# Optimization experiments

Hardware: AMD Instinct MI355X
Metric: run time of the kernel (lower is better)

## Reference

```python
import jax, jax.numpy as jnp
import numpy as np

N, E, D = 20000, 640000, 128  # nodes, edges, hidden_nf
ED = 3  # edge_feat_nf (1 input col + distance col + geodesic col)
NORM_FACTOR = 100.0
NORM_CONST = 1.0
LN_EPS = 1e-5


def setup_inputs() -> dict:
    key = jax.random.key(0)
    ks = jax.random.split(key, 24)
    w = lambda k, s: (jax.random.normal(k, s, dtype=jnp.float32) * 0.1)
    inp = {
        "h": jax.random.normal(ks[0], (N, D), dtype=jnp.float32),
        "x": jax.random.normal(ks[1], (N, 3), dtype=jnp.float32),
        "edge_index": jax.random.randint(ks[2], (2, E), 0, N),
        "node_mask": jnp.ones((N, 1), jnp.float32),
        "edge_mask": jnp.ones((E, 1), jnp.float32),
        "edge_attr": jax.random.uniform(ks[3], (E, 1), dtype=jnp.float32),
        # GCLayer params
        "W_lin": w(ks[4], (D, D)), "b_lin": jnp.zeros((D,), jnp.float32),
        "We1": w(ks[5], (D + ED, D)), "be1": jnp.zeros((D,), jnp.float32),
        "We2": w(ks[6], (D, D)), "be2": jnp.zeros((D,), jnp.float32),
        "Wn1": w(ks[7], (D, D)), "bn1": jnp.zeros((D,), jnp.float32),
        "Wn2": w(ks[8], (D, D)), "bn2": jnp.zeros((D,), jnp.float32),
        "Wa1": w(ks[9], (2 * D + ED, D)), "ba1": jnp.zeros((D,), jnp.float32),
        "Wa2": w(ks[10], (D, 1)), "ba2": jnp.zeros((1,), jnp.float32),
        "ln_g": jnp.ones((D,), jnp.float32), "ln_b": jnp.zeros((D,), jnp.float32),
        # EquivariantUpdate coord_mlp params (last layer bias-free, gain 0.001)
        "Wc1": w(ks[11], (2 * D + ED, D)), "bc1": jnp.zeros((D,), jnp.float32),
        "Wc2": w(ks[12], (D, D)), "bc2": jnp.zeros((D,), jnp.float32),
        "Wc3": w(ks[13], (D, 1)) * 0.01,
    }
    return inp


def _forward(h, x, edge_index, node_mask, edge_mask, edge_attr,
             W_lin, b_lin, We1, be1, We2, be2, Wn1, bn1, Wn2, bn2,
             Wa1, ba1, Wa2, ba2, ln_g, ln_b, Wc1, bc1, Wc2, bc2, Wc3):
    silu = jax.nn.silu
    row, col = edge_index[0], edge_index[1]
    # coord2diff
    diff = x[row] - x[col]                                     # [E,3]
    radial = jnp.sum(diff * diff, axis=1, keepdims=True)
    dist = jnp.sqrt(radial + 1e-8)                             # [E,1]
    coord_diff = diff / (dist + NORM_CONST)
    e = jnp.concatenate([dist, edge_attr], axis=1)             # [E,2]
    # ---- GCLayer (Euclidean reduction of HGCLayer) ----
    hh = h @ W_lin + b_lin                                     # [N,D]
    hr, hc = hh[row], hh[col]
    geo = jnp.sqrt(jnp.sum((hr - hc) ** 2, axis=1, keepdims=True) + 1e-8)
    e3 = jnp.concatenate([e, geo], axis=1)                     # [E,3]
    att_in = jnp.concatenate([hr, hc, e3], axis=1)             # [E,2D+3]
    att = jax.nn.sigmoid(silu(att_in @ Wa1 + ba1) @ Wa2 + ba2) * edge_mask
    msg_in = jnp.concatenate([hc - hr, e3], axis=1)            # [E,D+3]
    msg = (silu(msg_in @ We1 + be1) @ We2 + be2) * att
    agg = jax.ops.segment_sum(msg, row, num_segments=hh.shape[0])  # [N,D]
    out = silu(agg @ Wn1 + bn1) @ Wn2 + bn2
    hh = hh + out
    mu = jnp.mean(hh, axis=-1, keepdims=True)
    var = jnp.mean((hh - mu) ** 2, axis=-1, keepdims=True)
    hh = (hh - mu) * jax.lax.rsqrt(var + LN_EPS) * ln_g + ln_b
    hh = silu(hh)
    # ---- EquivariantUpdate (tanh=False) ----
    cin = jnp.concatenate([hh[row], hh[col], e3], axis=1)      # [E,2D+3]
    m = silu(cin @ Wc1 + bc1)
    m = silu(m @ Wc2 + bc2)
    m = m @ Wc3                                                # [E,1]
    trans = coord_diff * m * edge_mask
    aggx = jax.ops.segment_sum(trans, row, num_segments=x.shape[0]) / NORM_FACTOR
    x_out = (x + aggx) * node_mask
    return hh, x_out


def reference(h, x, edge_index, node_mask, edge_mask, edge_attr,
              W_lin, b_lin, We1, be1, We2, be2, Wn1, bn1, Wn2, bn2,
              Wa1, ba1, Wa2, ba2, ln_g, ln_b, Wc1, bc1, Wc2, bc2, Wc3):
    return _forward(h, x, edge_index, node_mask, edge_mask, edge_attr,
                    W_lin, b_lin, We1, be1, We2, be2, Wn1, bn1, Wn2, bn2,
                    Wa1, ba1, Wa2, ba2, ln_g, ln_b, Wc1, bc1, Wc2, bc2, Wc3)
```

## Files before the change

### kernel.cpp

```cpp
#include <hip/hip_runtime.h>
#include <hip/hip_bf16.h>


#define D 128
#define RS 136

typedef unsigned short ushort;
typedef __fp16 half8 __attribute__((ext_vector_type(8)));
typedef __fp16 h16x2 __attribute__((ext_vector_type(2)));
typedef _Float16 f16x2 __attribute__((ext_vector_type(2)));
typedef __attribute__((ext_vector_type(4))) float f32x4;

__device__ __forceinline__ float rcpf(float x) { return __builtin_amdgcn_rcpf(x); }
__device__ __forceinline__ float siluf(float x) { return x * rcpf(1.0f + __expf(-x)); }
__device__ __forceinline__ float sigmf(float x) { return rcpf(1.0f + __expf(-x)); }
__device__ __forceinline__ ushort f2hs(float f) {
    _Float16 h = (_Float16)f; ushort u; __builtin_memcpy(&u, &h, 2); return u;
}
__device__ __forceinline__ unsigned pkh(float lo, float hi) {
    auto h = __builtin_amdgcn_cvt_pkrtz(lo, hi);
    unsigned u; __builtin_memcpy(&u, &h, 4); return u;
}
__device__ __forceinline__ unsigned pkadd(unsigned a, unsigned b) {
    f16x2 x, y; __builtin_memcpy(&x, &a, 4); __builtin_memcpy(&y, &b, 4);
    f16x2 d = x + y; unsigned r; __builtin_memcpy(&r, &d, 4); return r;
}
__device__ __forceinline__ float2 up2(unsigned u) {
    f16x2 h; __builtin_memcpy(&h, &u, 4);
    return make_float2((float)h.x, (float)h.y);
}
__device__ __forceinline__ float fdot2f(f16x2 a, f16x2 b, float c) {
#if __has_builtin(__builtin_amdgcn_fdot2)
    h16x2 ah, bh;
    __builtin_memcpy(&ah, &a, 4); __builtin_memcpy(&bh, &b, 4);
    return __builtin_amdgcn_fdot2(ah, bh, c, false);
#else
    return c + (float)a.x * (float)b.x + (float)a.y * (float)b.y;
#endif
}
#define MFMA16(a, b, c) __builtin_amdgcn_mfma_f32_16x16x32_f16((a), (b), (c), 0, 0, 0)

#define PWLIN 0
#define PU    5
#define PV    9
#define PM    13
#define PE2   17
#define PN1   21
#define PN2   26
#define PP    30
#define PQ    34
#define PC2   38
#define NPACK 42

__global__ void k_zero(float* __restrict__ p, long n) {
    long i = (long)blockIdx.x * blockDim.x + threadIdx.x;
    long stride = (long)gridDim.x * blockDim.x;
    for (; i < n; i += stride) p[i] = 0.0f;
}

__global__ void k_hist(const int* __restrict__ eidx, int* __restrict__ cnt, int E) {
    int i = blockIdx.x * blockDim.x + threadIdx.x;
    const int stride = gridDim.x * blockDim.x;
    for (; i < E; i += stride) atomicAdd(&cnt[eidx[i]], 1);
}

__global__ __launch_bounds__(1024) void k_scan(const int* __restrict__ cnt,
                                               int* __restrict__ cur, int N) {
    __shared__ int part[1024];
    const int t = threadIdx.x;
    const int chunk = (N + 1023) / 1024;
    int s = 0;
    for (int k = 0; k < chunk; ++k) {
        const int i = t * chunk + k;
        if (i < N) s += cnt[i];
    }
    part[t] = s;
    __syncthreads();
    for (int d = 1; d < 1024; d <<= 1) {
        const int v = (t >= d) ? part[t - d] : 0;
        __syncthreads();
        part[t] += v;
        __syncthreads();
    }
    int base = (t == 0) ? 0 : part[t - 1];
    for (int k = 0; k < chunk; ++k) {
        const int i = t * chunk + k;
        if (i < N) { cur[i] = base; base += cnt[i]; }
    }
}

__global__ void k_scatter_build(
    const int* __restrict__ eidx, const float* __restrict__ x,
    const float* __restrict__ eattr, const float* __restrict__ emask,
    int* __restrict__ cur, float4* __restrict__ rec, int E) {
    int i = blockIdx.x * blockDim.x + threadIdx.x;
    const int stride = gridDim.x * blockDim.x;
    for (; i < E; i += stride) {
        const int r = eidx[i], c = eidx[E + i];
        const int p = atomicAdd(&cur[r], 1);
        const float dx = x[r * 3 + 0] - x[c * 3 + 0];
        const float dy = x[r * 3 + 1] - x[c * 3 + 1];
        const float dz = x[r * 3 + 2] - x[c * 3 + 2];
        const float dist = sqrtf(dx * dx + dy * dy + dz * dz + 1e-8f);
        const float inv = rcpf(dist + 1.0f);
        rec[2 * p + 0] = make_float4(__int_as_float(r), __int_as_float(c), dist, eattr[i]);
        rec[2 * p + 1] = make_float4(emask[i], dx * inv, dy * inv, dz * inv);
    }
}

__global__ __launch_bounds__(256) void k_packall(
    const float* __restrict__ W_lin, const float* __restrict__ b_lin,
    const float* __restrict__ Wa1,
    const float* __restrict__ We1,
    const float* __restrict__ We2,
    const float* __restrict__ Wn1, const float* __restrict__ bn1,
    const float* __restrict__ Wn2,
    const float* __restrict__ Wc1,
    const float* __restrict__ Wc2,
    ushort* __restrict__ pack) {
    const int b = blockIdx.x, t = threadIdx.x;
    const float* W = nullptr; const float* bias = nullptr;
    int kbase = 0, fold = 0, ext = 0, nW = 0;
    if (b < 5)       { W = W_lin; bias = b_lin; if (b == 4) { ext = 1; nW = 0; } else kbase = b * 32; }
    else if (b < 9)  { W = Wa1; kbase = (b - 5) * 32; }
    else if (b < 13) { W = Wa1; kbase = 128 + (b - 9) * 32; }
    else if (b < 17) { W = We1; kbase = (b - 13) * 32; }
    else if (b < 21) { W = We2; kbase = (b - 17) * 32; }
    else if (b < 26) { int k = b - 21; W = Wn1; bias = bn1; if (k == 4) { ext = 1; nW = 0; } else kbase = k * 32; }
    else if (b < 30) { W = Wn2; kbase = (b - 26) * 32; }
    else if (b < 34) { W = Wc1; kbase = (b - 30) * 32; }
    else if (b < 38) { W = Wc1; kbase = 128 + (b - 34) * 32; }
    else             { W = Wc2; kbase = (b - 38) * 32; }
    ushort* dst = pack + (size_t)b * 4096;
#pragma unroll
    for (int i = 0; i < 16; ++i) {
        const int e = t + 256 * i;
        const int j = e & 7, lane = (e >> 3) & 63, nt = e >> 9;
        const int kl = (lane >> 4) * 8 + j;
        const int n = nt * 16 + (lane & 15);
        float v;
        if (!ext) {
            v = W[(kbase + kl) * D + n];
            if (fold) v += W[(kbase + kl + 128) * D + n];
        } else {
            v = (kl < nW) ? W[(kbase + kl) * D + n] : (kl == nW ? bias[n] : 0.0f);
        }
        dst[e] = f2hs(v);
    }
}

__global__ __launch_bounds__(256) void k_node_lin(
    const float* __restrict__ h, const ushort* __restrict__ pack,
    float* __restrict__ hh, ushort* __restrict__ hh1b,
    ushort* __restrict__ Vp, ushort* __restrict__ Vh,
    ushort* __restrict__ Mp, ushort* __restrict__ Mh,
    const float* __restrict__ ba1f, const float* __restrict__ be1f, int N) {
    __shared__ ushort hs[64][RS];
    const int t = threadIdx.x, lane = t & 63, wave = t >> 6;
    const int quad = lane >> 4, l16 = lane & 15;
    const int mh = wave >> 1, nh = wave & 1;
    const int base = blockIdx.x * 64;

#pragma unroll
    for (int q = 0; q < 8; ++q) {
        const int f = t + 256 * q;
        const int row = f >> 5, c4 = (f & 31) << 2;
        const int node = base + row;
        float4 v = make_float4(0.f, 0.f, 0.f, 0.f);
        if (node < N) v = *(const float4*)(h + (size_t)node * D + c4);
        *(uint2*)&hs[row][c4] = make_uint2(pkh(v.x, v.y), pkh(v.z, v.w));
    }
    float ba1v[4], be1v[4];
#pragma unroll
    for (int nt = 0; nt < 4; ++nt) {
        const int col = nh * 64 + nt * 16 + l16;
        ba1v[nt] = ba1f[col]; be1v[nt] = be1f[col];
    }
    __syncthreads();

    half8 aext = (half8)0;
    if (quad == 0) aext[0] = (__fp16)1.0f;

    f32x4 acc[2][4] = {};
    {
        const half8* pB = (const half8*)(pack + (size_t)PWLIN * 4096);
#pragma unroll
        for (int ks = 0; ks < 5; ++ks) {
            half8 bfr[4];
#pragma unroll
            for (int nt = 0; nt < 4; ++nt) bfr[nt] = pB[(ks * 8 + nh * 4 + nt) * 64 + lane];
#pragma unroll
            for (int mt = 0; mt < 2; ++mt) {
                const half8 a = (ks < 4) ? *(const half8*)&hs[mh * 32 + mt * 16 + l16][ks * 32 + quad * 8]
                                         : aext;
#pragma unroll
                for (int nt = 0; nt < 4; ++nt) acc[mt][nt] = MFMA16(a, bfr[nt], acc[mt][nt]);
            }
        }
    }
    __syncthreads();
#pragma unroll
    for (int mt = 0; mt < 2; ++mt)
#pragma unroll
        for (int reg = 0; reg < 4; ++reg) {
            const int row = mh * 32 + mt * 16 + quad * 4 + reg;
            const int g = base + row;
#pragma unroll
            for (int nt = 0; nt < 4; ++nt) {
                const int col = nh * 64 + nt * 16 + l16;
                const float v = acc[mt][nt][reg];
                const ushort hv = f2hs(v);
                hs[row][col] = hv;
                if (g < N) {
                    hh[(size_t)g * D + col] = v;
                    hh1b[(size_t)g * D + col] = hv;
                }
            }
        }
    __syncthreads();

    {
        f32x4 a2[2][4] = {};
        const half8* pB = (const half8*)(pack + (size_t)PU * 4096);
#pragma unroll
        for (int ks = 0; ks < 4; ++ks) {
            half8 bfr[4];
#pragma unroll
            for (int nt = 0; nt < 4; ++nt) bfr[nt] = pB[(ks * 8 + nh * 4 + nt) * 64 + lane];
#pragma unroll
            for (int mt = 0; mt < 2; ++mt) {
                const half8 a = *(const half8*)&hs[mh * 32 + mt * 16 + l16][ks * 32 + quad * 8];
#pragma unroll
                for (int nt = 0; nt < 4; ++nt) a2[mt][nt] = MFMA16(a, bfr[nt], a2[mt][nt]);
            }
        }
#pragma unroll
        for (int mt = 0; mt < 2; ++mt)
#pragma unroll
            for (int reg = 0; reg < 4; ++reg) {
                const int g = base + mh * 32 + mt * 16 + quad * 4 + reg;
                if (g < N)
#pragma unroll
                    for (int nt = 0; nt < 4; ++nt)
                        Vp[(size_t)g * D + nh * 64 + nt * 16 + l16] = f2hs(a2[mt][nt][reg] + ba1v[nt]);
            }
    }
    {
        f32x4 a2[2][4] = {};
        const half8* pB = (const half8*)(pack + (size_t)PV * 4096);
#pragma unroll
        for (int ks = 0; ks < 4; ++ks) {
            half8 bfr[4];
#pragma unroll
            for (int nt = 0; nt < 4; ++nt) bfr[nt] = pB[(ks * 8 + nh * 4 + nt) * 64 + lane];
#pragma unroll
            for (int mt = 0; mt < 2; ++mt) {
                const half8 a = *(const half8*)&hs[mh * 32 + mt * 16 + l16][ks * 32 + quad * 8];
#pragma unroll
                for (int nt = 0; nt < 4; ++nt) a2[mt][nt] = MFMA16(a, bfr[nt], a2[mt][nt]);
            }
        }
#pragma unroll
        for (int mt = 0; mt < 2; ++mt)
#pragma unroll
            for (int reg = 0; reg < 4; ++reg) {
                const int g = base + mh * 32 + mt * 16 + quad * 4 + reg;
                if (g < N)
#pragma unroll
                    for (int nt = 0; nt < 4; ++nt)
                        Vh[(size_t)g * D + nh * 64 + nt * 16 + l16] = f2hs(a2[mt][nt][reg]);
            }
    }
    {
        f32x4 a2[2][4] = {};
        const half8* pB = (const half8*)(pack + (size_t)PM * 4096);
#pragma unroll
        for (int ks = 0; ks < 4; ++ks) {
            half8 bfr[4];
#pragma unroll
            for (int nt = 0; nt < 4; ++nt) bfr[nt] = pB[(ks * 8 + nh * 4 + nt) * 64 + lane];
#pragma unroll
            for (int mt = 0; mt < 2; ++mt) {
                const half8 a = *(const half8*)&hs[mh * 32 + mt * 16 + l16][ks * 32 + quad * 8];
#pragma unroll
                for (int nt = 0; nt < 4; ++nt) a2[mt][nt] = MFMA16(a, bfr[nt], a2[mt][nt]);
            }
        }
#pragma unroll
        for (int mt = 0; mt < 2; ++mt)
#pragma unroll
            for (int reg = 0; reg < 4; ++reg) {
                const int g = base + mh * 32 + mt * 16 + quad * 4 + reg;
                if (g < N)
#pragma unroll
                    for (int nt = 0; nt < 4; ++nt) {
                        const int col = nh * 64 + nt * 16 + l16;
                        const float v = a2[mt][nt][reg];
                        Mh[(size_t)g * D + col] = f2hs(v);
                        Mp[(size_t)g * D + col] = f2hs(be1v[nt] - v);
                    }
            }
    }
}

__global__ __launch_bounds__(256, 6) void k_edge1(
    const float4* __restrict__ rec,
    const ushort* __restrict__ hh1b,
    const ushort* __restrict__ Vp, const ushort* __restrict__ Vh,
    const ushort* __restrict__ Mp, const ushort* __restrict__ Mh,
    const ushort* __restrict__ pack,
    const float* __restrict__ Wa1, const float* __restrict__ We1,
    const float* __restrict__ Wa2f, const float* __restrict__ ba2f,
    const float* __restrict__ be2f,
    float* __restrict__ agg, float* __restrict__ geo_c, int E) {
    __shared__ ushort m1_s[64][RS];
    __shared__ float ew_s[7][128];
    __shared__ float dist_s[64], attr_s[64], geo_s[64], att_s[64], em_s[64];
    __shared__ int node_s[64], col_s[64];

    float (*msg_s)[RS] = (float(*)[RS])&m1_s[0][0];

    const int t = threadIdx.x, lane = t & 63, w = t >> 6;
    const int quad = lane >> 4, l16 = lane & 15;
    const int base = blockIdx.x * 64;

    if (t < 64) {
        const int i = base + t;
        int r = 0, c = 0; float dist = 0.f, at = 0.f, emv = 0.f;
        if (i < E) {
            const float4 ra = rec[2 * i + 0];
            const float4 rb = rec[2 * i + 1];
            r = __float_as_int(ra.x); c = __float_as_int(ra.y);
            dist = ra.z; at = ra.w; emv = rb.x;
        }
        node_s[t] = r; col_s[t] = c;
        dist_s[t] = dist; attr_s[t] = at; em_s[t] = emv;
    }
    for (int i = t; i < 896; i += 256) {
        const int r = i >> 7, c = i & 127;
        float v;
        if (r < 3)      v = Wa1[(256 + r) * D + c];
        else if (r < 6) v = We1[(128 + (r - 3)) * D + c];
        else            v = Wa2f[c];
        ew_s[r][c] = v;
    }
    float b3[2];
#pragma unroll
    for (int nt = 0; nt < 2; ++nt) b3[nt] = be2f[w * 32 + nt * 16 + l16];
    __syncthreads();

    {
        const int g = t >> 4;
#pragma unroll
        for (int it = 0; it < 4; ++it) {
            const int e = g * 4 + it;
            const uint4 vr = *(const uint4*)(hh1b + (size_t)node_s[e] * D + l16 * 8);
            const uint4 vc = *(const uint4*)(hh1b + (size_t)col_s[e] * D + l16 * 8);
            const unsigned* pr = (const unsigned*)&vr;
            const unsigned* pc = (const unsigned*)&vc;
            float s = 0.f;
#pragma unroll
            for (int q = 0; q < 4; ++q) {
                f16x2 hr2, hc2;
                __builtin_memcpy(&hr2, &pr[q], 4);
                __builtin_memcpy(&hc2, &pc[q], 4);
                const f16x2 d2 = hc2 - hr2;
                s = fdot2f(d2, d2, s);
            }
            s += __shfl_xor(s, 1); s += __shfl_xor(s, 2); s += __shfl_xor(s, 4); s += __shfl_xor(s, 8);
            if (l16 == 0) {
                const float gg = sqrtf(s + 1e-8f);
                geo_s[e] = gg;
                if (base + e < E) geo_c[base + e] = gg;
            }
        }
    }
    __syncthreads();

    {
        const int row = t >> 2, cq = t & 3;
        const int nr = node_s[row], nc = col_s[row];
        const float dist = dist_s[row], attr = attr_s[row], geo = geo_s[row];
        const ushort* pVr = Vp + (size_t)nr * D + cq * 32;
        const ushort* pVc = Vh + (size_t)nc * D + cq * 32;
        const ushort* pMr = Mp + (size_t)nr * D + cq * 32;
        const ushort* pMc = Mh + (size_t)nc * D + cq * 32;
        float p = 0.f;
#pragma unroll
        for (int k4 = 0; k4 < 8; ++k4) {
            const int c4 = cq * 32 + k4 * 4;
            const uint2 vru = *(const uint2*)(pVr + k4 * 4);
            const uint2 vcu = *(const uint2*)(pVc + k4 * 4);
            const uint2 mru = *(const uint2*)(pMr + k4 * 4);
            const uint2 mcu = *(const uint2*)(pMc + k4 * 4);
            const float2 av01 = up2(pkadd(vru.x, vcu.x));
            const float2 av23 = up2(pkadd(vru.y, vcu.y));
            const float2 mv01 = up2(pkadd(mru.x, mcu.x));
            const float2 mv23 = up2(pkadd(mru.y, mcu.y));
            const float4 e0 = *(const float4*)&ew_s[0][c4];
            const float4 e1 = *(const float4*)&ew_s[1][c4];
            const float4 e2 = *(const float4*)&ew_s[2][c4];
            const float4 f0 = *(const float4*)&ew_s[3][c4];
            const float4 f1 = *(const float4*)&ew_s[4][c4];
            const float4 f2 = *(const float4*)&ew_s[5][c4];
            const float4 w2 = *(const float4*)&ew_s[6][c4];
            const float a0 = av01.x + dist * e0.x + attr * e1.x + geo * e2.x;
            const float a1 = av01.y + dist * e0.y + attr * e1.y + geo * e2.y;
            const float a2 = av23.x + dist * e0.z + attr * e1.z + geo * e2.z;
            const float a3 = av23.y + dist * e0.w + attr * e1.w + geo * e2.w;
            p += siluf(a0) * w2.x + siluf(a1) * w2.y + siluf(a2) * w2.z + siluf(a3) * w2.w;
            const float m0 = siluf(mv01.x + dist * f0.x + attr * f1.x + geo * f2.x);
            const float m1v = siluf(mv01.y + dist * f0.y + attr * f1.y + geo * f2.y);
            const float m2 = siluf(mv23.x + dist * f0.z + attr * f1.z + geo * f2.z);
            const float m3 = siluf(mv23.y + dist * f0.w + attr * f1.w + geo * f2.w);
            *(uint2*)&m1_s[row][c4] = make_uint2(pkh(m0, m1v), pkh(m2, m3));
        }
        p += __shfl_xor(p, 1); p += __shfl_xor(p, 2);
        if (cq == 0) att_s[row] = sigmf(p + ba2f[0]) * em_s[row];
    }
    __syncthreads();

    f32x4 acc3[4][2] = {};
    {
        const half8* pB = (const half8*)(pack + (size_t)PE2 * 4096);
#pragma unroll
        for (int ks = 0; ks < 4; ++ks) {
            const half8 b0 = pB[(ks * 8 + w * 2 + 0) * 64 + lane];
            const half8 b1 = pB[(ks * 8 + w * 2 + 1) * 64 + lane];
#pragma unroll
            for (int mt = 0; mt < 4; ++mt) {
                const half8 a = *(const half8*)&m1_s[mt * 16 + l16][ks * 32 + quad * 8];
                acc3[mt][0] = MFMA16(a, b0, acc3[mt][0]);
                acc3[mt][1] = MFMA16(a, b1, acc3[mt][1]);
            }
        }
    }
    __syncthreads();

#pragma unroll
    for (int pass = 0; pass < 2; ++pass) {
#pragma unroll
        for (int mt = 0; mt < 2; ++mt)
#pragma unroll
            for (int reg = 0; reg < 4; ++reg) {
                const int row = (pass * 2 + mt) * 16 + quad * 4 + reg;
                const float av = att_s[row];
#pragma unroll
                for (int nt = 0; nt < 2; ++nt)
                    msg_s[row - pass * 32][w * 32 + nt * 16 + l16] =
                        (acc3[pass * 2 + mt][nt][reg] + b3[nt]) * av;
            }
        __syncthreads();
        {
            const int j = t & 127, s = t >> 7;
            const int r0 = pass * 32 + s * 16;
            float acc = 0.f;
            int rprev = node_s[r0];
#pragma unroll
            for (int k = 0; k < 16; ++k) {
                const int rn = node_s[r0 + k];
                if (rn != rprev) {
                    atomicAdd(&agg[(size_t)rprev * D + j], acc);
                    acc = 0.f; rprev = rn;
                }
                acc += msg_s[s * 16 + k][j];
            }
            atomicAdd(&agg[(size_t)rprev * D + j], acc);
        }
        __syncthreads();
    }
}

__global__ __launch_bounds__(256) void k_node2(
    const float* __restrict__ agg, float* hio,
    const ushort* __restrict__ pack,
    const float* __restrict__ bn2f,
    const float* __restrict__ ln_g, const float* __restrict__ ln_b,
    const float* __restrict__ bc1f,
    ushort* __restrict__ Ph, ushort* __restrict__ Qh, int N) {
    __shared__ ushort ag_s[64][RS];
    __shared__ float redS[2][64], redQ[2][64];
    const int t = threadIdx.x, lane = t & 63, wave = t >> 6;
    const int quad = lane >> 4, l16 = lane & 15;
    const int mh = wave >> 1, nh = wave & 1;
    const int base = blockIdx.x * 64;

#pragma unroll
    for (int q = 0; q < 8; ++q) {
        const int f = t + 256 * q;
        const int row = f >> 5, c4 = (f & 31) << 2;
        const int node = base + row;
        float4 v = make_float4(0.f, 0.f, 0.f, 0.f);
        if (node < N) v = *(const float4*)(agg + (size_t)node * D + c4);
        *(uint2*)&ag_s[row][c4] = make_uint2(pkh(v.x, v.y), pkh(v.z, v.w));
    }
    float bn2[4], lg[4], lb[4], bc1v[4];
#pragma unroll
    for (int nt = 0; nt < 4; ++nt) {
        const int col = nh * 64 + nt * 16 + l16;
        bn2[nt] = bn2f[col]; lg[nt] = ln_g[col]; lb[nt] = ln_b[col]; bc1v[nt] = bc1f[col];
    }
    __syncthreads();

    half8 aext = (half8)0;
    if (quad == 0) aext[0] = (__fp16)1.0f;

    f32x4 acc[2][4] = {};
    {
        const half8* pB = (const half8*)(pack + (size_t)PN1 * 4096);
#pragma unroll
        for (int ks = 0; ks < 5; ++ks) {
            half8 bfr[4];
#pragma unroll
            for (int nt = 0; nt < 4; ++nt) bfr[nt] = pB[(ks * 8 + nh * 4 + nt) * 64 + lane];
#pragma unroll
            for (int mt = 0; mt < 2; ++mt) {
                const half8 a = (ks < 4) ? *(const half8*)&ag_s[mh * 32 + mt * 16 + l16][ks * 32 + quad * 8]
                                         : aext;
#pragma unroll
                for (int nt = 0; nt < 4; ++nt) acc[mt][nt] = MFMA16(a, bfr[nt], acc[mt][nt]);
            }
        }
    }
    __syncthreads();
#pragma unroll
    for (int mt = 0; mt < 2; ++mt)
#pragma unroll
        for (int reg = 0; reg < 4; ++reg) {
            const int row = mh * 32 + mt * 16 + quad * 4 + reg;
#pragma unroll
            for (int nt = 0; nt < 4; ++nt)
                ag_s[row][nh * 64 + nt * 16 + l16] = f2hs(siluf(acc[mt][nt][reg]));
        }
    __syncthreads();

    {
        const half8* pB = (const half8*)(pack + (size_t)PN2 * 4096);
#pragma unroll
        for (int mt = 0; mt < 2; ++mt)
#pragma unroll
            for (int nt = 0; nt < 4; ++nt) acc[mt][nt] = (f32x4)0.0f;
#pragma unroll
        for (int ks = 0; ks < 4; ++ks) {
            half8 bfr[4];
#pragma unroll
            for (int nt = 0; nt < 4; ++nt) bfr[nt] = pB[(ks * 8 + nh * 4 + nt) * 64 + lane];
#pragma unroll
            for (int mt = 0; mt < 2; ++mt) {
                const half8 a = *(const half8*)&ag_s[mh * 32 + mt * 16 + l16][ks * 32 + quad * 8];
#pragma unroll
                for (int nt = 0; nt < 4; ++nt) acc[mt][nt] = MFMA16(a, bfr[nt], acc[mt][nt]);
            }
        }
    }
#pragma unroll
    for (int mt = 0; mt < 2; ++mt)
#pragma unroll
        for (int reg = 0; reg < 4; ++reg) {
            const int row = mh * 32 + mt * 16 + quad * 4 + reg;
            const int g = base + row;
            float s = 0.f, qq = 0.f;
#pragma unroll
            for (int nt = 0; nt < 4; ++nt) {
                const int col = nh * 64 + nt * 16 + l16;
                float v = acc[mt][nt][reg] + bn2[nt];
                if (g < N) v += hio[(size_t)g * D + col];
                acc[mt][nt][reg] = v;
                s += v; qq += v * v;
            }
            s += __shfl_xor(s, 1); s += __shfl_xor(s, 2); s += __shfl_xor(s, 4); s += __shfl_xor(s, 8);
            qq += __shfl_xor(qq, 1); qq += __shfl_xor(qq, 2); qq += __shfl_xor(qq, 4); qq += __shfl_xor(qq, 8);
            if (l16 == 0) { redS[nh][row] = s; redQ[nh][row] = qq; }
        }
    __syncthreads();

#pragma unroll
    for (int mt = 0; mt < 2; ++mt)
#pragma unroll
        for (int reg = 0; reg < 4; ++reg) {
            const int row = mh * 32 + mt * 16 + quad * 4 + reg;
            const int g = base + row;
            const float mu = (redS[0][row] + redS[1][row]) * (1.0f / D);
            const float var = (redQ[0][row] + redQ[1][row]) * (1.0f / D) - mu * mu;
            const float rstd = rsqrtf(var + 1e-5f);
#pragma unroll
            for (int nt = 0; nt < 4; ++nt) {
                const int col = nh * 64 + nt * 16 + l16;
                const float hn = (acc[mt][nt][reg] - mu) * rstd * lg[nt] + lb[nt];
                const float o = siluf(hn);
                ag_s[row][col] = f2hs(o);
                if (g < N) hio[(size_t)g * D + col] = o;
            }
        }
    __syncthreads();

    {
        f32x4 a2[2][4] = {};
        const half8* pB = (const half8*)(pack + (size_t)PP * 4096);
#pragma unroll
        for (int ks = 0; ks < 4; ++ks) {
            half8 bfr[4];
#pragma unroll
            for (int nt = 0; nt < 4; ++nt) bfr[nt] = pB[(ks * 8 + nh * 4 + nt) * 64 + lane];
#pragma unroll
            for (int mt = 0; mt < 2; ++mt) {
                const half8 a = *(const half8*)&ag_s[mh * 32 + mt * 16 + l16][ks * 32 + quad * 8];
#pragma unroll
                for (int nt = 0; nt < 4; ++nt) a2[mt][nt] = MFMA16(a, bfr[nt], a2[mt][nt]);
            }
        }
#pragma unroll
        for (int mt = 0; mt < 2; ++mt)
#pragma unroll
            for (int reg = 0; reg < 4; ++reg) {
                const int g = base + mh * 32 + mt * 16 + quad * 4 + reg;
                if (g < N)
#pragma unroll
                    for (int nt = 0; nt < 4; ++nt)
                        Ph[(size_t)g * D + nh * 64 + nt * 16 + l16] = f2hs(a2[mt][nt][reg] + bc1v[nt]);
            }
    }
    {
        f32x4 a2[2][4] = {};
        const half8* pB = (const half8*)(pack + (size_t)PQ * 4096);
#pragma unroll
        for (int ks = 0; ks < 4; ++ks) {
            half8 bfr[4];
#pragma unroll
            for (int nt = 0; nt < 4; ++nt) bfr[nt] = pB[(ks * 8 + nh * 4 + nt) * 64 + lane];
#pragma unroll
            for (int mt = 0; mt < 2; ++mt) {
                const half8 a = *(const half8*)&ag_s[mh * 32 + mt * 16 + l16][ks * 32 + quad * 8];
#pragma unroll
                for (int nt = 0; nt < 4; ++nt) a2[mt][nt] = MFMA16(a, bfr[nt], a2[mt][nt]);
            }
        }
#pragma unroll
        for (int mt = 0; mt < 2; ++mt)
#pragma unroll
            for (int reg = 0; reg < 4; ++reg) {
                const int g = base + mh * 32 + mt * 16 + quad * 4 + reg;
                if (g < N)
#pragma unroll
                    for (int nt = 0; nt < 4; ++nt)
                        Qh[(size_t)g * D + nh * 64 + nt * 16 + l16] = f2hs(a2[mt][nt][reg]);
            }
    }
}

__global__ __launch_bounds__(256, 6) void k_edge2(
    const float4* __restrict__ rec, const float* __restrict__ geo_c,
    const ushort* __restrict__ Ph, const ushort* __restrict__ Qh,
    const ushort* __restrict__ pack,
    const float* __restrict__ Wc1,
    const float* __restrict__ bc2f, const float* __restrict__ Wc3f,
    float* __restrict__ aggx, int E) {
    __shared__ ushort c1_s[64][RS];
    __shared__ float ew_s[3][128];
    __shared__ float dist_s[64], attr_s[64], geo_s[64], tr_s[64];
    __shared__ float cdx_s[64], cdy_s[64], cdz_s[64];
    __shared__ int node_s[64], col_s[64];
    __shared__ float mp_s[4][64];

    const int t = threadIdx.x, lane = t & 63, w = t >> 6;
    const int quad = lane >> 4, l16 = lane & 15;
    const int base = blockIdx.x * 64;

    if (t < 64) {
        const int i = base + t;
        int r = 0, c = 0;
        float dist = 1.f, geo = 0.f, at = 0.f, emv = 0.f, cdx = 0.f, cdy = 0.f, cdz = 0.f;
        if (i < E) {
            const float4 ra = rec[2 * i + 0];
            const float4 rb = rec[2 * i + 1];
            r = __float_as_int(ra.x); c = __float_as_int(ra.y);
            dist = ra.z; at = ra.w;
            emv = rb.x; cdx = rb.y; cdy = rb.z; cdz = rb.w;
            geo = geo_c[i];
        }
        node_s[t] = r; col_s[t] = c;
        dist_s[t] = dist; geo_s[t] = geo; attr_s[t] = at; tr_s[t] = emv;
        cdx_s[t] = cdx; cdy_s[t] = cdy; cdz_s[t] = cdz;
    }
    for (int i = t; i < 384; i += 256) {
        const int r = i >> 7, c = i & 127;
        ew_s[r][c] = Wc1[(256 + r) * D + c];
    }
    float bc2[2], wc3[2];
#pragma unroll
    for (int nt = 0; nt < 2; ++nt) {
        const int col = w * 32 + nt * 16 + l16;
        bc2[nt] = bc2f[col]; wc3[nt] = Wc3f[col];
    }
    __syncthreads();

    {
        const int row = t >> 2, cq = t & 3;
        const int nr = node_s[row], nc = col_s[row];
        const float dist = dist_s[row], attr = attr_s[row], geo = geo_s[row];
        const ushort* pP = Ph + (size_t)nr * D + cq * 32;
        const ushort* pQ = Qh + (size_t)nc * D + cq * 32;
#pragma unroll
        for (int k4 = 0; k4 < 8; ++k4) {
            const int c4 = cq * 32 + k4 * 4;
            const uint2 pu = *(const uint2*)(pP + k4 * 4);
            const uint2 qu = *(const uint2*)(pQ + k4 * 4);
            const float2 s01 = up2(pkadd(pu.x, qu.x));
            const float2 s23 = up2(pkadd(pu.y, qu.y));
            const float4 e0 = *(const float4*)&ew_s[0][c4];
            const float4 e1 = *(const float4*)&ew_s[1][c4];
            const float4 e2 = *(const float4*)&ew_s[2][c4];
            const float c0 = siluf(s01.x + dist * e0.x + attr * e1.x + geo * e2.x);
            const float c1 = siluf(s01.y + dist * e0.y + attr * e1.y + geo * e2.y);
            const float c2 = siluf(s23.x + dist * e0.z + attr * e1.z + geo * e2.z);
            const float c3 = siluf(s23.y + dist * e0.w + attr * e1.w + geo * e2.w);
            *(uint2*)&c1_s[row][c4] = make_uint2(pkh(c0, c1), pkh(c2, c3));
        }
    }
    __syncthreads();

    {
        f32x4 acc[4][2] = {};
        const half8* pB = (const half8*)(pack + (size_t)PC2 * 4096);
#pragma unroll
        for (int ks = 0; ks < 4; ++ks) {
            const half8 b0 = pB[(ks * 8 + w * 2 + 0) * 64 + lane];
            const half8 b1 = pB[(ks * 8 + w * 2 + 1) * 64 + lane];
#pragma unroll
            for (int mt = 0; mt < 4; ++mt) {
                const half8 a = *(const half8*)&c1_s[mt * 16 + l16][ks * 32 + quad * 8];
                acc[mt][0] = MFMA16(a, b0, acc[mt][0]);
                acc[mt][1] = MFMA16(a, b1, acc[mt][1]);
            }
        }
#pragma unroll
        for (int mt = 0; mt < 4; ++mt)
#pragma unroll
            for (int reg = 0; reg < 4; ++reg) {
                float p = siluf(acc[mt][0][reg] + bc2[0]) * wc3[0]
                        + siluf(acc[mt][1][reg] + bc2[1]) * wc3[1];
                p += __shfl_xor(p, 1); p += __shfl_xor(p, 2); p += __shfl_xor(p, 4); p += __shfl_xor(p, 8);
                if (l16 == 0) mp_s[w][mt * 16 + quad * 4 + reg] = p;
            }
    }
    __syncthreads();

    if (t < 64) {
        const float m = mp_s[0][t] + mp_s[1][t] + mp_s[2][t] + mp_s[3][t];
        tr_s[t] = m * tr_s[t];
        if (base + t >= E) tr_s[t] = 0.f;
    }
    __syncthreads();

    {
        const int h = t >> 7, tt = t & 127;
        if (tt < 3) {
            const float* cds = (tt == 0) ? cdx_s : (tt == 1) ? cdy_s : cdz_s;
            float acc = 0.f;
            int rprev = node_s[h * 32];
#pragma unroll
            for (int k = 0; k < 32; ++k) {
                const int row = h * 32 + k;
                const int rn = node_s[row];
                if (rn != rprev) {
                    atomicAdd(&aggx[rprev * 4 + tt], acc);
                    acc = 0.f; rprev = rn;
                }
                acc += cds[row] * tr_s[row];
            }
            atomicAdd(&aggx[rprev * 4 + tt], acc);
        }
    }
}

__global__ void k_coord(const float* __restrict__ x, const float* __restrict__ nmask,
                        const float* __restrict__ aggx, float* __restrict__ out_x, int N) {
    const int idx = blockIdx.x * blockDim.x + threadIdx.x;
    if (idx >= N * 3) return;
    const int i = idx / 3, d = idx - i * 3;
    out_x[idx] = (x[idx] + aggx[i * 4 + d] * (1.0f / 100.0f)) * nmask[i];
}

extern "C" void kernel_launch(void* const* d_in, const int* in_sizes, int n_in,
                              void* d_out, int out_size, void* d_ws, size_t ws_size,
                              hipStream_t stream) {
    const float* h     = (const float*)d_in[0];
    const float* x     = (const float*)d_in[1];
    const int*   eidx  = (const int*)d_in[2];
    const float* nmask = (const float*)d_in[3];
    const float* emask = (const float*)d_in[4];
    const float* eattr = (const float*)d_in[5];
    const float* W_lin = (const float*)d_in[6];
    const float* b_lin = (const float*)d_in[7];
    const float* We1   = (const float*)d_in[8];
    const float* be1   = (const float*)d_in[9];
    const float* We2   = (const float*)d_in[10];
    const float* be2   = (const float*)d_in[11];
    const float* Wn1   = (const float*)d_in[12];
    const float* bn1   = (const float*)d_in[13];
    const float* Wn2   = (const float*)d_in[14];
    const float* bn2   = (const float*)d_in[15];
    const float* Wa1   = (const float*)d_in[16];
    const float* ba1   = (const float*)d_in[17];
    const float* Wa2   = (const float*)d_in[18];
    const float* ba2   = (const float*)d_in[19];
    const float* ln_g  = (const float*)d_in[20];
    const float* ln_b  = (const float*)d_in[21];
    const float* Wc1   = (const float*)d_in[22];
    const float* bc1   = (const float*)d_in[23];
    const float* Wc2   = (const float*)d_in[24];
    const float* bc2   = (const float*)d_in[25];
    const float* Wc3   = (const float*)d_in[26];

    const int N = in_sizes[0] / D;
    const int E = in_sizes[2] / 2;

    char* wp = (char*)d_ws;
    auto take = [&](size_t bytes) -> void* {
        void* p = wp; wp += (bytes + 255) & ~(size_t)255; return p;
    };
    float*  agg   = (float*)take((size_t)N * D * 4);
    float*  aggx  = (float*)take((size_t)N * 4 * 4);
    int*    cnt   = (int*)take((size_t)N * 4);
    int*    cur   = (int*)take((size_t)N * 4);
    float4* rec   = (float4*)take((size_t)E * 32);
    float*  geo_c = (float*)take((size_t)E * 4);
    ushort* hh1b  = (ushort*)take((size_t)N * D * 2);
    ushort* Vp    = (ushort*)take((size_t)N * D * 2);
    ushort* Vh    = (ushort*)take((size_t)N * D * 2);
    ushort* Mp    = (ushort*)take((size_t)N * D * 2);
    ushort* Mh    = (ushort*)take((size_t)N * D * 2);
    ushort* Ph    = (ushort*)take((size_t)N * D * 2);
    ushort* Qh    = (ushort*)take((size_t)N * D * 2);
    ushort* pack  = (ushort*)take((size_t)NPACK * 4096 * 2);

    float* out_h = (float*)d_out;
    float* out_x = out_h + (size_t)N * D;

    const int EB = (E + 63) / 64;
    const int NB = (N + 63) / 64;
    const long zn = ((char*)(cnt + N) - (char*)agg) / 4;

    k_zero<<<2048, 256, 0, stream>>>(agg, zn);
    k_packall<<<NPACK, 256, 0, stream>>>(W_lin, b_lin, Wa1, We1, We2,
                                         Wn1, bn1, Wn2, Wc1, Wc2, pack);
    k_hist<<<1024, 256, 0, stream>>>(eidx, cnt, E);
    k_scan<<<1, 1024, 0, stream>>>(cnt, cur, N);
    k_scatter_build<<<1024, 256, 0, stream>>>(eidx, x, eattr, emask, cur, rec, E);
    k_node_lin<<<NB, 256, 0, stream>>>(h, pack, out_h, hh1b, Vp, Vh, Mp, Mh, ba1, be1, N);
    k_edge1<<<EB, 256, 0, stream>>>(rec, hh1b, Vp, Vh, Mp, Mh, pack, Wa1, We1,
                                    Wa2, ba2, be2, agg, geo_c, E);
    k_node2<<<NB, 256, 0, stream>>>(agg, out_h, pack, bn2, ln_g, ln_b, bc1, Ph, Qh, N);
    k_edge2<<<EB, 256, 0, stream>>>(rec, geo_c, Ph, Qh, pack, Wc1, bc2, Wc3, aggx, E);
    k_coord<<<(N * 3 + 255) / 256, 256, 0, stream>>>(x, nmask, aggx, out_x, N);
}
```

Measured before the change: 460.9 us.

## Move edge-MLP second layer after aggregation using linearity of segment sum

The second edge-MLP matmul (We2) is linear, so the sum over edges of att*(m1@We2+be2) equals (sum of att*m1)@We2 + (sum of att)*be2. The edge kernel now scatters att-weighted first-layer activations plus a per-node attention sum, and the node kernel applies We2 and the bias once per node. This removes an E-sized MFMA GEMM and its LDS staging, in exchange for an extra N-sized GEMM, an extra atomic per edge and a second fp16 rounding of the aggregated sum before We2.

```diff
diff --git a/kernel.cpp b/kernel.cpp
--- a/kernel.cpp
+++ b/kernel.cpp
@@ -308,20 +308,16 @@
     const ushort* __restrict__ hh1b,
     const ushort* __restrict__ Vp, const ushort* __restrict__ Vh,
     const ushort* __restrict__ Mp, const ushort* __restrict__ Mh,
-    const ushort* __restrict__ pack,
     const float* __restrict__ Wa1, const float* __restrict__ We1,
     const float* __restrict__ Wa2f, const float* __restrict__ ba2f,
-    const float* __restrict__ be2f,
-    float* __restrict__ agg, float* __restrict__ geo_c, int E) {
-    __shared__ ushort m1_s[64][RS];
+    float* __restrict__ s1, float* __restrict__ satt,
+    float* __restrict__ geo_c, int E) {
+    __shared__ float msg_s[32][RS];
     __shared__ float ew_s[7][128];
     __shared__ float dist_s[64], attr_s[64], geo_s[64], att_s[64], em_s[64];
     __shared__ int node_s[64], col_s[64];
 
-    float (*msg_s)[RS] = (float(*)[RS])&m1_s[0][0];
-
-    const int t = threadIdx.x, lane = t & 63, w = t >> 6;
-    const int quad = lane >> 4, l16 = lane & 15;
+    const int t = threadIdx.x;
     const int base = blockIdx.x * 64;
 
     if (t < 64) {
@@ -344,12 +340,10 @@
         else            v = Wa2f[c];
         ew_s[r][c] = v;
     }
-    float b3[2];
-#pragma unroll
-    for (int nt = 0; nt < 2; ++nt) b3[nt] = be2f[w * 32 + nt * 16 + l16];
-    __syncthreads();
-
-    {
+    __syncthreads();
+
+    {
+        const int l16 = t & 15;
         const int g = t >> 4;
 #pragma unroll
         for (int it = 0; it < 4; ++it) {
@@ -377,8 +371,9 @@
     }
     __syncthreads();
 
-    {
-        const int row = t >> 2, cq = t & 3;
+    unsigned msil[16];
+    const int row = t >> 2, cq = t & 3;
+    {
         const int nr = node_s[row], nc = col_s[row];
         const float dist = dist_s[row], attr = attr_s[row], geo = geo_s[row];
         const ushort* pVr = Vp + (size_t)nr * D + cq * 32;
@@ -413,43 +408,30 @@
             const float m1v = siluf(mv01.y + dist * f0.y + attr * f1.y + geo * f2.y);
             const float m2 = siluf(mv23.x + dist * f0.z + attr * f1.z + geo * f2.z);
             const float m3 = siluf(mv23.y + dist * f0.w + attr * f1.w + geo * f2.w);
-            *(uint2*)&m1_s[row][c4] = make_uint2(pkh(m0, m1v), pkh(m2, m3));
+            msil[k4 * 2 + 0] = pkh(m0, m1v);
+            msil[k4 * 2 + 1] = pkh(m2, m3);
         }
         p += __shfl_xor(p, 1); p += __shfl_xor(p, 2);
         if (cq == 0) att_s[row] = sigmf(p + ba2f[0]) * em_s[row];
     }
     __syncthreads();
 
-    f32x4 acc3[4][2] = {};
-    {
-        const half8* pB = (const half8*)(pack + (size_t)PE2 * 4096);
-#pragma unroll
-        for (int ks = 0; ks < 4; ++ks) {
-            const half8 b0 = pB[(ks * 8 + w * 2 + 0) * 64 + lane];
-            const half8 b1 = pB[(ks * 8 + w * 2 + 1) * 64 + lane];
-#pragma unroll
-            for (int mt = 0; mt < 4; ++mt) {
-                const half8 a = *(const half8*)&m1_s[mt * 16 + l16][ks * 32 + quad * 8];
-                acc3[mt][0] = MFMA16(a, b0, acc3[mt][0]);
-                acc3[mt][1] = MFMA16(a, b1, acc3[mt][1]);
-            }
-        }
-    }
-    __syncthreads();
+    if (t < 64 && base + t < E) atomicAdd(&satt[node_s[t]], att_s[t]);
 
 #pragma unroll
     for (int pass = 0; pass < 2; ++pass) {
-#pragma unroll
-        for (int mt = 0; mt < 2; ++mt)
-#pragma unroll
-            for (int reg = 0; reg < 4; ++reg) {
-                const int row = (pass * 2 + mt) * 16 + quad * 4 + reg;
-                const float av = att_s[row];
-#pragma unroll
-                for (int nt = 0; nt < 2; ++nt)
-                    msg_s[row - pass * 32][w * 32 + nt * 16 + l16] =
-                        (acc3[pass * 2 + mt][nt][reg] + b3[nt]) * av;
-            }
+        if ((row >> 5) == pass) {
+            const float av = att_s[row];
+            const int lr = row & 31;
+#pragma unroll
+            for (int k4 = 0; k4 < 8; ++k4) {
+                const int c4 = cq * 32 + k4 * 4;
+                const float2 m01 = up2(msil[k4 * 2 + 0]);
+                const float2 m23 = up2(msil[k4 * 2 + 1]);
+                *(float4*)&msg_s[lr][c4] =
+                    make_float4(m01.x * av, m01.y * av, m23.x * av, m23.y * av);
+            }
+        }
         __syncthreads();
         {
             const int j = t & 127, s = t >> 7;
@@ -460,20 +442,22 @@
             for (int k = 0; k < 16; ++k) {
                 const int rn = node_s[r0 + k];
                 if (rn != rprev) {
-                    atomicAdd(&agg[(size_t)rprev * D + j], acc);
+                    atomicAdd(&s1[(size_t)rprev * D + j], acc);
                     acc = 0.f; rprev = rn;
                 }
                 acc += msg_s[s * 16 + k][j];
             }
-            atomicAdd(&agg[(size_t)rprev * D + j], acc);
+            atomicAdd(&s1[(size_t)rprev * D + j], acc);
         }
         __syncthreads();
     }
 }
 
 __global__ __launch_bounds__(256) void k_node2(
-    const float* __restrict__ agg, float* hio,
+    const float* __restrict__ s1, const float* __restrict__ satt,
+    float* hio,
     const ushort* __restrict__ pack,
+    const float* __restrict__ be2f,
     const float* __restrict__ bn2f,
     const float* __restrict__ ln_g, const float* __restrict__ ln_b,
     const float* __restrict__ bc1f,
@@ -491,14 +475,15 @@
         const int row = f >> 5, c4 = (f & 31) << 2;
         const int node = base + row;
         float4 v = make_float4(0.f, 0.f, 0.f, 0.f);
-        if (node < N) v = *(const float4*)(agg + (size_t)node * D + c4);
+        if (node < N) v = *(const float4*)(s1 + (size_t)node * D + c4);
         *(uint2*)&ag_s[row][c4] = make_uint2(pkh(v.x, v.y), pkh(v.z, v.w));
     }
-    float bn2[4], lg[4], lb[4], bc1v[4];
+    float bn2[4], lg[4], lb[4], bc1v[4], be2v[4];
 #pragma unroll
     for (int nt = 0; nt < 4; ++nt) {
         const int col = nh * 64 + nt * 16 + l16;
-        bn2[nt] = bn2f[col]; lg[nt] = ln_g[col]; lb[nt] = ln_b[col]; bc1v[nt] = bc1f[col];
+        bn2[nt] = bn2f[col]; lg[nt] = ln_g[col]; lb[nt] = ln_b[col];
+        bc1v[nt] = bc1f[col]; be2v[nt] = be2f[col];
     }
     __syncthreads();
 
@@ -507,7 +492,42 @@
 
     f32x4 acc[2][4] = {};
     {
+        const half8* pB = (const half8*)(pack + (size_t)PE2 * 4096);
+#pragma unroll
+        for (int ks = 0; ks < 4; ++ks) {
+            half8 bfr[4];
+#pragma unroll
+            for (int nt = 0; nt < 4; ++nt) bfr[nt] = pB[(ks * 8 + nh * 4 + nt) * 64 + lane];
+#pragma unroll
+            for (int mt = 0; mt < 2; ++mt) {
+                const half8 a = *(const half8*)&ag_s[mh * 32 + mt * 16 + l16][ks * 32 + quad * 8];
+#pragma unroll
+                for (int nt = 0; nt < 4; ++nt) acc[mt][nt] = MFMA16(a, bfr[nt], acc[mt][nt]);
+            }
+        }
+    }
+    __syncthreads();
+#pragma unroll
+    for (int mt = 0; mt < 2; ++mt)
+#pragma unroll
+        for (int reg = 0; reg < 4; ++reg) {
+            const int row = mh * 32 + mt * 16 + quad * 4 + reg;
+            const int g = base + row;
+            const float sa = (g < N) ? satt[g] : 0.f;
+#pragma unroll
+            for (int nt = 0; nt < 4; ++nt) {
+                const float v = acc[mt][nt][reg] + sa * be2v[nt];
+                ag_s[row][nh * 64 + nt * 16 + l16] = f2hs(v);
+            }
+        }
+    __syncthreads();
+
+    {
         const half8* pB = (const half8*)(pack + (size_t)PN1 * 4096);
+#pragma unroll
+        for (int mt = 0; mt < 2; ++mt)
+#pragma unroll
+            for (int nt = 0; nt < 4; ++nt) acc[mt][nt] = (f32x4)0.0f;
 #pragma unroll
         for (int ks = 0; ks < 5; ++ks) {
             half8 bfr[4];
@@ -819,8 +839,9 @@
     auto take = [&](size_t bytes) -> void* {
         void* p = wp; wp += (bytes + 255) & ~(size_t)255; return p;
     };
-    float*  agg   = (float*)take((size_t)N * D * 4);
+    float*  s1    = (float*)take((size_t)N * D * 4);
     float*  aggx  = (float*)take((size_t)N * 4 * 4);
+    float*  satt  = (float*)take((size_t)N * 4);
     int*    cnt   = (int*)take((size_t)N * 4);
     int*    cur   = (int*)take((size_t)N * 4);
     float4* rec   = (float4*)take((size_t)E * 32);
@@ -839,18 +860,19 @@
 
     const int EB = (E + 63) / 64;
     const int NB = (N + 63) / 64;
-    const long zn = ((char*)(cnt + N) - (char*)agg) / 4;
-
-    k_zero<<<2048, 256, 0, stream>>>(agg, zn);
+    const long zn = ((char*)(cnt + N) - (char*)s1) / 4;
+
+    k_zero<<<2048, 256, 0, stream>>>(s1, zn);
     k_packall<<<NPACK, 256, 0, stream>>>(W_lin, b_lin, Wa1, We1, We2,
                                          Wn1, bn1, Wn2, Wc1, Wc2, pack);
     k_hist<<<1024, 256, 0, stream>>>(eidx, cnt, E);
     k_scan<<<1, 1024, 0, stream>>>(cnt, cur, N);
     k_scatter_build<<<1024, 256, 0, stream>>>(eidx, x, eattr, emask, cur, rec, E);
     k_node_lin<<<NB, 256, 0, stream>>>(h, pack, out_h, hh1b, Vp, Vh, Mp, Mh, ba1, be1, N);
-    k_edge1<<<EB, 256, 0, stream>>>(rec, hh1b, Vp, Vh, Mp, Mh, pack, Wa1, We1,
-                                    Wa2, ba2, be2, agg, geo_c, E);
-    k_node2<<<NB, 256, 0, stream>>>(agg, out_h, pack, bn2, ln_g, ln_b, bc1, Ph, Qh, N);
+    k_edge1<<<EB, 256, 0, stream>>>(rec, hh1b, Vp, Vh, Mp, Mh, Wa1, We1,
+                                    Wa2, ba2, s1, satt, geo_c, E);
+    k_node2<<<NB, 256, 0, stream>>>(s1, satt, out_h, pack, be2, bn2, ln_g, ln_b,
+                                    bc1, Ph, Qh, N);
     k_edge2<<<EB, 256, 0, stream>>>(rec, geo_c, Ph, Qh, pack, Wc1, bc2, Wc3, aggx, E);
     k_coord<<<(N * 3 + 255) / 256, 256, 0, stream>>>(x, nmask, aggx, out_x, N);
 }
```

Measured after the change: 675.8 us. 1.47x slower.
